# Kernel optimization log

Measured on AMD Instinct MI355X. Metric: run time of the kernel, lower is better.

Reference implementation:

```python
import jax, jax.numpy as jnp
import numpy as np

B, T, C, U = 256, 1024, 128, 100   # batch, time, num_classes (incl. blank), max label len
BLANK = C - 1                      # TF/Keras CTC: blank is the LAST class
NEG = -1.0e30                      # log-space -inf surrogate (fp32-safe)
EPS = 1e-7                         # keras backend epsilon used in ctc_batch_cost


def setup_inputs() -> dict:
    key = jax.random.key(0)
    k1, k2, k3 = jax.random.split(key, 3)
    # ctc_batch_cost consumes post-softmax probabilities
    logits = jax.random.normal(k1, (B, T, C), dtype=jnp.float32)
    y_pred = jax.nn.softmax(logits, axis=-1)
    y_true = jax.random.randint(k2, (B, U), 0, BLANK)          # labels in [0, C-2]
    label_len = jax.random.randint(k3, (B,), 1, U + 1)         # 1..U
    return {"y_pred": y_pred, "y_true": y_true, "label_len": label_len}


def _ctc_batch_cost(y_pred, y_true, label_len):
    # log probs, matching keras: log(prob + epsilon)
    logp = jnp.log(y_pred + EPS)                               # [B,T,C]
    S = 2 * U + 1
    # extended label sequence: blank, l1, blank, l2, ..., blank
    ext = jnp.full((B, S), BLANK, dtype=y_true.dtype)
    ext = ext.at[:, 1::2].set(y_true)                          # [B,S]
    # skip (s-2 -> s) allowed iff ext[s] != blank and ext[s] != ext[s-2]
    can_skip = jnp.concatenate(
        [jnp.zeros((B, 2), dtype=bool),
         (ext[:, 2:] != BLANK) & (ext[:, 2:] != ext[:, :-2])], axis=1)  # [B,S]

    logp_t = jnp.transpose(logp, (1, 0, 2))                    # [T,B,C]
    # t = 0 init: only s=0 (blank) and s=1 (first label) reachable
    lp0 = jnp.take_along_axis(logp_t[0], ext, axis=1)          # [B,S]
    alpha0 = jnp.full((B, S), NEG, dtype=logp.dtype)
    alpha0 = alpha0.at[:, 0].set(lp0[:, 0]).at[:, 1].set(lp0[:, 1])

    def step(alpha, lp_c):
        # lp_c: [B,C] log probs at time t; gather per extended-label position
        lp = jnp.take_along_axis(lp_c, ext, axis=1)            # [B,S]
        a1 = jnp.pad(alpha[:, :-1], ((0, 0), (1, 0)), constant_values=NEG)
        a2 = jnp.pad(alpha[:, :-2], ((0, 0), (2, 0)), constant_values=NEG)
        a2 = jnp.where(can_skip, a2, NEG)
        alpha = jax.nn.logsumexp(jnp.stack([alpha, a1, a2]), axis=0) + lp
        return alpha, None

    alpha, _ = jax.lax.scan(step, alpha0, logp_t[1:])          # [B,S]
    # total log-likelihood ends at s = 2L-1 (last label) or s = 2L (trailing blank)
    end = 2 * label_len[:, None]                               # [B,1]
    a_end = jnp.take_along_axis(alpha, jnp.concatenate([end - 1, end], axis=1), axis=1)
    return -jax.nn.logsumexp(a_end, axis=1, keepdims=True)     # [B,1] per-example loss


def reference(y_pred, y_true, label_len):
    # matches tf.keras.backend.ctc_batch_cost(y_true, y_pred, fill(T), label_len)
    return _ctc_batch_cost(y_pred, y_true, label_len)
```

## Files before the change

kernel.cpp:

```cpp
#include <hip/hip_runtime.h>


#define Bc 256
#define Tc 1024
#define Cc 128
#define Uc 100
#define BLANKc 127
#define EPSc 1e-7f
#define LN2f 0.69314718055994530942f
#define RSTRIDE 130
#define NSLOT 128
#define SLOTB (NSLOT*RSTRIDE*4)
#define QD 8

__global__ __launch_bounds__(64) void ctc_skew_kernel(
    const float* __restrict__ y_pred,
    const int*   __restrict__ y_true,
    const int*   __restrict__ label_len,
    float*       __restrict__ out)
{
    __shared__ __align__(16) float rowbuf[NSLOT * RSTRIDE];
    __shared__ float shA[204];
    __shared__ int   shE[64];

    const int b    = blockIdx.x;
    const int lane = threadIdx.x;
    const float* gp = y_pred + (size_t)b * (Tc * Cc);
    char* rb = (char*)rowbuf;

    const int k0  = 2*lane, k1 = 2*lane+1;
    const int k0c = k0 < Uc ? k0 : Uc-1;
    const int k1c = k1 < Uc ? k1 : Uc-1;
    const int y0  = y_true[b*Uc + k0c];
    const int y1  = y_true[b*Uc + k1c];
    int ym1 = y0;
    if (lane > 0) ym1 = y_true[b*Uc + k0 - 1];
    const float ms1 = (lane > 0 && y0 != ym1) ? 1.0f : 0.0f;
    const float ms3 = (y1 != y0) ? 1.0f : 0.0f;
    const float mh  = (lane > 0) ? 1.0f : 0.0f;
    const int y0b = y0 * 4, y1b = y1 * 4;

    float a0=0.f, a1=0.f, a2=0.f, a3=0.f;
    if (lane == 0) { a0 = gp[BLANKc]+EPSc; a1 = gp[y0]+EPSc; }
    int e = 0;

    {
        const float4 z = make_float4(0.f, 0.f, 0.f, 0.f);
        float4* rb4 = (float4*)rowbuf;
#pragma unroll
        for (int i = 0; i < 65; ++i) rb4[i*64 + lane] = z;
    }

#pragma unroll
    for (int i = 0; i < 8; ++i) {
        const int f4  = i*64 + lane;
        const int row = f4 >> 5;
        const int c4  = (f4 & 31) * 4;
        float4 v = *(const float4*)(gp + row*Cc + c4);
        float* dst = &rowbuf[row*RSTRIDE + c4];
        dst[0]=v.x+EPSc; dst[1]=v.y+EPSc; dst[2]=v.z+EPSc; dst[3]=v.w+EPSc;
    }

    float2 Q[QD];
#pragma unroll
    for (int k = 0; k < QD; ++k)
        Q[k] = *(const float2*)(gp + (16+k)*Cc + lane*2);

    int swb = (((1 - lane) & (NSLOT-1)) * RSTRIDE - RSTRIDE) * 4;
    if (swb < 0) swb += SLOTB;
    int wswb = 15 * RSTRIDE * 4;
    const int lane8 = lane * 8;

    float q2a = 0.f, q1a = 0.f;
    int ELa = 0, ELb = 0;

    auto body = [&](int n, int j, bool fzp) {
        swb += RSTRIDE*4; if (swb >= SLOTB) swb -= SLOTB;
        const float pb = *(const float*)(rb + swb + BLANKc*4);
        const float p0 = *(const float*)(rb + swb + y0b);
        const float p1 = *(const float*)(rb + swb + y1b);
        wswb += RSTRIDE*4; if (wswb >= SLOTB) wswb -= SLOTB;
        float2 qv = Q[j & 7];
        qv.x += EPSc; qv.y += EPSc;
        *(float2*)(rb + wswb + lane8) = qv;
        int lr = n + 23; lr = lr > Tc-1 ? Tc-1 : lr;
        Q[j & 7] = *(const float2*)(gp + lr*Cc + lane*2);
        const int el = ((j == 0) || (j >= 5 && j <= 8) || (j >= 13)) ? ELb : ELa;
        const float h1r = q2a; q2a = q1a;
        int d = el - e; d = d > 126 ? 126 : d;
        const float h1 = mh * ldexpf(h1r, d);
        const float n0 = (a0 + h1) * pb;
        const float n1 = (a1 + a0 + ms1*h1) * p0;
        const float n2 = (a2 + a1) * pb;
        const float n3 = (a3 + a2 + ms3*a1) * p1;
        bool upd = true;
        if (fzp) upd = (lane >= n - (Tc-1));
        if (upd) { a0=n0; a1=n1; a2=n2; a3=n3; }
        if ((j & 3) == 3) {
            const float m = fmaxf(fmaxf(a0,a1), fmaxf(a2,a3));
            int ex = (int)((__float_as_uint(m) >> 23) & 0xFF) - 127;
            ex = (m > 0.0f) ? ex : (el - e);
            a0 = ldexpf(a0,-ex); a1 = ldexpf(a1,-ex);
            a2 = ldexpf(a2,-ex); a3 = ldexpf(a3,-ex);
            e += ex;
        }
        q1a = __shfl_up(a3, 1, 64);
        if ((j & 3) == 3) {
            const int es = __shfl_up(e, 1, 64);
            if (j == 3 || j == 11) ELb = es; else ELa = es;
        }
    };

    int n = 1;
    for (int c = 0; c < 63; ++c) {
#pragma unroll
        for (int j = 0; j < 16; ++j) { body(n, j, false); ++n; }
    }
    for (int c = 0; c < 4; ++c) {
#pragma unroll
        for (int j = 0; j < 16; ++j) { body(n, j, true); ++n; }
    }
    body(n, 0, true);

    if (lane < 51) {
        shA[4*lane+0] = a0; shA[4*lane+1] = a1;
        shA[4*lane+2] = a2; shA[4*lane+3] = a3;
        shE[lane] = e;
    }
    __syncthreads();
    if (lane == 0) {
        const int L  = label_len[b];
        const int s1 = 2*L - 1, s2 = 2*L;
        const float v1 = shA[s1], v2 = shA[s2];
        const int   e1 = shE[s1 >> 2], e2 = shE[s2 >> 2];
        const int   em = e1 > e2 ? e1 : e2;
        const float sum = ldexpf(v1, e1-em) + ldexpf(v2, e2-em);
        const float r   = __log2f(sum) + (float)em;
        out[b] = -LN2f * r;
    }
}

extern "C" void kernel_launch(void* const* d_in, const int* in_sizes, int n_in,
                              void* d_out, int out_size, void* d_ws, size_t ws_size,
                              hipStream_t stream) {
    const float* y_pred    = (const float*)d_in[0];
    const int*   y_true    = (const int*)d_in[1];
    const int*   label_len = (const int*)d_in[2];
    float*       out       = (float*)d_out;
    ctc_skew_kernel<<<Bc, 64, 0, stream>>>(y_pred, y_true, label_len, out);
}
```

Before: 252.0 us.

## Process two time steps per iteration with a two-step lane skew

The wavefront schedule changes so that each lane lags its neighbour by two time steps instead of one. Each iteration then computes two recurrence steps back to back, with one cross-lane shuffle between them, and renormalises once per pair. The exponent and shifted-alpha history registers are restructured to match. The row ring buffer grows to 160 slots and the prefetch queue to 16 rows to cover the larger skew. This aims to halve per-step shuffle, exponent and ring-index overhead on the serial dependency chain, at the cost of more LDS, more registers and a longer drain phase.

```diff
diff --git a/kernel.cpp b/kernel.cpp
--- a/kernel.cpp
+++ b/kernel.cpp
@@ -9,11 +9,12 @@
 #define EPSc 1e-7f
 #define LN2f 0.69314718055994530942f
 #define RSTRIDE 130
-#define NSLOT 128
-#define SLOTB (NSLOT*RSTRIDE*4)
-#define QD 8
+#define NSLOT 160
+#define RSB (RSTRIDE*4)
+#define SLOTB (NSLOT*RSB)
+#define QD 16
 
-__global__ __launch_bounds__(64) void ctc_skew_kernel(
+__global__ __launch_bounds__(64) void ctc_pair_kernel(
     const float* __restrict__ y_pred,
     const int*   __restrict__ y_true,
     const int*   __restrict__ label_len,
@@ -39,20 +40,22 @@
     const float ms3 = (y1 != y0) ? 1.0f : 0.0f;
     const float mh  = (lane > 0) ? 1.0f : 0.0f;
     const int y0b = y0 * 4, y1b = y1 * 4;
+    const int lane2 = lane * 2, lane8 = lane * 8;
 
     float a0=0.f, a1=0.f, a2=0.f, a3=0.f;
     if (lane == 0) { a0 = gp[BLANKc]+EPSc; a1 = gp[y0]+EPSc; }
     int e = 0;
 
     {
-        const float4 z = make_float4(0.f, 0.f, 0.f, 0.f);
+        const float4 z = make_float4(0.f,0.f,0.f,0.f);
         float4* rb4 = (float4*)rowbuf;
 #pragma unroll
-        for (int i = 0; i < 65; ++i) rb4[i*64 + lane] = z;
+        for (int i = 0; i < 81; ++i) rb4[i*64 + lane] = z;
+        if (lane < 16) rb4[81*64 + lane] = z;
     }
 
 #pragma unroll
-    for (int i = 0; i < 8; ++i) {
+    for (int i = 0; i < 9; ++i) {
         const int f4  = i*64 + lane;
         const int row = f4 >> 5;
         const int c4  = (f4 & 31) * 4;
@@ -64,39 +67,61 @@
     float2 Q[QD];
 #pragma unroll
     for (int k = 0; k < QD; ++k)
-        Q[k] = *(const float2*)(gp + (16+k)*Cc + lane*2);
+        Q[k] = *(const float2*)(gp + (18+k)*Cc + lane2);
 
-    int swb = (((1 - lane) & (NSLOT-1)) * RSTRIDE - RSTRIDE) * 4;
-    if (swb < 0) swb += SLOTB;
-    int wswb = 15 * RSTRIDE * 4;
-    const int lane8 = lane * 8;
+    int r0 = 1 - lane2; r0 %= NSLOT; if (r0 < 0) r0 += NSLOT;
+    int sprev = r0*RSB - RSB; if (sprev < 0) sprev += SLOTB;
+    int wprev = 16*RSB;
+    int n2 = 2;
 
-    float q2a = 0.f, q1a = 0.f;
-    int ELa = 0, ELb = 0;
+    float hA1 = 0.f, hB1 = 0.f, hB2 = 0.f;
+    int   eL1 = 0,   eL2 = 0;
 
-    auto body = [&](int n, int j, bool fzp) {
-        swb += RSTRIDE*4; if (swb >= SLOTB) swb -= SLOTB;
-        const float pb = *(const float*)(rb + swb + BLANKc*4);
-        const float p0 = *(const float*)(rb + swb + y0b);
-        const float p1 = *(const float*)(rb + swb + y1b);
-        wswb += RSTRIDE*4; if (wswb >= SLOTB) wswb -= SLOTB;
-        float2 qv = Q[j & 7];
-        qv.x += EPSc; qv.y += EPSc;
-        *(float2*)(rb + wswb + lane8) = qv;
-        int lr = n + 23; lr = lr > Tc-1 ? Tc-1 : lr;
-        Q[j & 7] = *(const float2*)(gp + lr*Cc + lane*2);
-        const int el = ((j == 0) || (j >= 5 && j <= 8) || (j >= 13)) ? ELb : ELa;
-        const float h1r = q2a; q2a = q1a;
+    auto iter = [&](int j, bool fzp) {
+        int s1 = sprev + RSB; if (s1 >= SLOTB) s1 -= SLOTB;
+        int s2 = s1 + RSB;    if (s2 >= SLOTB) s2 -= SLOTB;
+        sprev = s2;
+        const float pb1 = *(const float*)(rb + s1 + BLANKc*4);
+        const float p01 = *(const float*)(rb + s1 + y0b);
+        const float p11 = *(const float*)(rb + s1 + y1b);
+        const float pb2 = *(const float*)(rb + s2 + BLANKc*4);
+        const float p02 = *(const float*)(rb + s2 + y0b);
+        const float p12 = *(const float*)(rb + s2 + y1b);
+        int w1 = wprev + 2*RSB; if (w1 >= SLOTB) w1 -= SLOTB;
+        int w2 = w1 + RSB;      if (w2 >= SLOTB) w2 -= SLOTB;
+        wprev = w1;
+        float2 qa = Q[2*j], qb = Q[2*j+1];
+        qa.x += EPSc; qa.y += EPSc; qb.x += EPSc; qb.y += EPSc;
+        *(float2*)(rb + w1 + lane8) = qa;
+        *(float2*)(rb + w2 + lane8) = qb;
+        int lr1 = n2 + 32; lr1 = lr1 > Tc-1 ? Tc-1 : lr1;
+        int lr2 = n2 + 33; lr2 = lr2 > Tc-1 ? Tc-1 : lr2;
+        Q[2*j]   = *(const float2*)(gp + lr1*Cc + lane2);
+        Q[2*j+1] = *(const float2*)(gp + lr2*Cc + lane2);
+        const int el = eL2;
         int d = el - e; d = d > 126 ? 126 : d;
-        const float h1 = mh * ldexpf(h1r, d);
-        const float n0 = (a0 + h1) * pb;
-        const float n1 = (a1 + a0 + ms1*h1) * p0;
-        const float n2 = (a2 + a1) * pb;
-        const float n3 = (a3 + a2 + ms3*a1) * p1;
-        bool upd = true;
-        if (fzp) upd = (lane >= n - (Tc-1));
-        if (upd) { a0=n0; a1=n1; a2=n2; a3=n3; }
-        if ((j & 3) == 3) {
+        const float h1 = mh * ldexpf(hB2, d);
+        const float h2 = mh * ldexpf(hA1, d);
+        {
+            const float n0 = (a0 + h1) * pb1;
+            const float n1 = (a1 + a0 + ms1*h1) * p01;
+            const float nv = (a2 + a1) * pb1;
+            const float n3 = (a3 + a2 + ms3*a1) * p11;
+            bool upd = true;
+            if (fzp) upd = (lane2 >= n2 - 1024);
+            if (upd) { a0=n0; a1=n1; a2=nv; a3=n3; }
+        }
+        const float haNew = __shfl_up(a3, 1, 64);
+        {
+            const float n0 = (a0 + h2) * pb2;
+            const float n1 = (a1 + a0 + ms1*h2) * p02;
+            const float nv = (a2 + a1) * pb2;
+            const float n3 = (a3 + a2 + ms3*a1) * p12;
+            bool upd = true;
+            if (fzp) upd = (lane2 >= n2 - 1023);
+            if (upd) { a0=n0; a1=n1; a2=nv; a3=n3; }
+        }
+        {
             const float m = fmaxf(fmaxf(a0,a1), fmaxf(a2,a3));
             int ex = (int)((__float_as_uint(m) >> 23) & 0xFF) - 127;
             ex = (m > 0.0f) ? ex : (el - e);
@@ -104,23 +129,20 @@
             a2 = ldexpf(a2,-ex); a3 = ldexpf(a3,-ex);
             e += ex;
         }
-        q1a = __shfl_up(a3, 1, 64);
-        if ((j & 3) == 3) {
-            const int es = __shfl_up(e, 1, 64);
-            if (j == 3 || j == 11) ELb = es; else ELa = es;
-        }
+        hB2 = hB1; hB1 = __shfl_up(a3, 1, 64);
+        eL2 = eL1; eL1 = __shfl_up(e , 1, 64);
+        hA1 = haNew;
+        n2 += 2;
     };
 
-    int n = 1;
     for (int c = 0; c < 63; ++c) {
 #pragma unroll
-        for (int j = 0; j < 16; ++j) { body(n, j, false); ++n; }
+        for (int j = 0; j < 8; ++j) iter(j, false);
     }
-    for (int c = 0; c < 4; ++c) {
+    for (int c = 0; c < 8; ++c) {
 #pragma unroll
-        for (int j = 0; j < 16; ++j) { body(n, j, true); ++n; }
+        for (int j = 0; j < 8; ++j) iter(j, true);
     }
-    body(n, 0, true);
 
     if (lane < 51) {
         shA[4*lane+0] = a0; shA[4*lane+1] = a1;
@@ -147,5 +169,5 @@
     const int*   y_true    = (const int*)d_in[1];
     const int*   label_len = (const int*)d_in[2];
     float*       out       = (float*)d_out;
-    ctc_skew_kernel<<<Bc, 64, 0, stream>>>(y_pred, y_true, label_len, out);
+    ctc_pair_kernel<<<Bc, 64, 0, stream>>>(y_pred, y_true, label_len, out);
 }
```

Result: slower. 271.0 us (+7.6%).

## Gather per-lane label probabilities directly from global into compact LDS ring

Applied to the files above, without the earlier changes.

Instead of staging whole probability rows in shared memory and gathering three columns per step from LDS, each lane now gathers its blank/y0/y1 probabilities from global memory 16 rows ahead and stores them as a float4 in a per-lane slot ring. Reads from the ring are skewed by lane and prefetched 4 steps ahead into registers, so LDS traffic per step drops to one float4 write and one read. This trades coalesced float2 row loads for scattered 4-byte global gathers, uses more registers for the 16-deep queue, and replaces the two-register shuffle history with a 16-entry array.

```diff
diff --git a/kernel.cpp b/kernel.cpp
--- a/kernel.cpp
+++ b/kernel.cpp
@@ -8,25 +8,22 @@
 #define BLANKc 127
 #define EPSc 1e-7f
 #define LN2f 0.69314718055994530942f
-#define RSTRIDE 130
-#define NSLOT 128
-#define SLOTB (NSLOT*RSTRIDE*4)
-#define QD 8
+#define SLOTS 128
+#define QGD 16
 
-__global__ __launch_bounds__(64) void ctc_skew_kernel(
+__global__ __launch_bounds__(64) void ctc_vg_kernel(
     const float* __restrict__ y_pred,
     const int*   __restrict__ y_true,
     const int*   __restrict__ label_len,
     float*       __restrict__ out)
 {
-    __shared__ __align__(16) float rowbuf[NSLOT * RSTRIDE];
-    __shared__ float shA[204];
-    __shared__ int   shE[64];
+    __shared__ float4 pbuf[SLOTS][64];
+    __shared__ float  shA[204];
+    __shared__ int    shE[64];
 
     const int b    = blockIdx.x;
     const int lane = threadIdx.x;
     const float* gp = y_pred + (size_t)b * (Tc * Cc);
-    char* rb = (char*)rowbuf;
 
     const int k0  = 2*lane, k1 = 2*lane+1;
     const int k0c = k0 < Uc ? k0 : Uc-1;
@@ -38,64 +35,56 @@
     const float ms1 = (lane > 0 && y0 != ym1) ? 1.0f : 0.0f;
     const float ms3 = (y1 != y0) ? 1.0f : 0.0f;
     const float mh  = (lane > 0) ? 1.0f : 0.0f;
-    const int y0b = y0 * 4, y1b = y1 * 4;
 
     float a0=0.f, a1=0.f, a2=0.f, a3=0.f;
     if (lane == 0) { a0 = gp[BLANKc]+EPSc; a1 = gp[y0]+EPSc; }
     int e = 0;
 
-    {
-        const float4 z = make_float4(0.f, 0.f, 0.f, 0.f);
-        float4* rb4 = (float4*)rowbuf;
+    const float4 z4 = make_float4(0.f,0.f,0.f,0.f);
+    for (int s = 64; s < SLOTS; ++s) pbuf[s][lane] = z4;
+
+    for (int r = 0; r < 5; ++r) {
+        const float* rp = gp + r*Cc;
+        pbuf[r][lane] = make_float4(rp[BLANKc], rp[y0], rp[y1], 0.f);
+    }
+    float4 QG[QGD];
 #pragma unroll
-        for (int i = 0; i < 65; ++i) rb4[i*64 + lane] = z;
+    for (int k = 0; k < QGD; ++k) QG[k] = z4;
+    for (int r = 5; r <= 16; ++r) {
+        const float* rp = gp + r*Cc;
+        QG[r & 15] = make_float4(rp[BLANKc], rp[y0], rp[y1], 0.f);
     }
+    float4 PQ[4];
+#pragma unroll
+    for (int nc = 1; nc <= 4; ++nc)
+        PQ[nc & 3] = pbuf[(nc - lane) & (SLOTS-1)][lane];
 
+    float HQ[16];
 #pragma unroll
-    for (int i = 0; i < 8; ++i) {
-        const int f4  = i*64 + lane;
-        const int row = f4 >> 5;
-        const int c4  = (f4 & 31) * 4;
-        float4 v = *(const float4*)(gp + row*Cc + c4);
-        float* dst = &rowbuf[row*RSTRIDE + c4];
-        dst[0]=v.x+EPSc; dst[1]=v.y+EPSc; dst[2]=v.z+EPSc; dst[3]=v.w+EPSc;
-    }
-
-    float2 Q[QD];
-#pragma unroll
-    for (int k = 0; k < QD; ++k)
-        Q[k] = *(const float2*)(gp + (16+k)*Cc + lane*2);
-
-    int swb = (((1 - lane) & (NSLOT-1)) * RSTRIDE - RSTRIDE) * 4;
-    if (swb < 0) swb += SLOTB;
-    int wswb = 15 * RSTRIDE * 4;
-    const int lane8 = lane * 8;
-
-    float q2a = 0.f, q1a = 0.f;
+    for (int k = 0; k < 16; ++k) HQ[k] = 0.f;
     int ELa = 0, ELb = 0;
 
     auto body = [&](int n, int j, bool fzp) {
-        swb += RSTRIDE*4; if (swb >= SLOTB) swb -= SLOTB;
-        const float pb = *(const float*)(rb + swb + BLANKc*4);
-        const float p0 = *(const float*)(rb + swb + y0b);
-        const float p1 = *(const float*)(rb + swb + y1b);
-        wswb += RSTRIDE*4; if (wswb >= SLOTB) wswb -= SLOTB;
-        float2 qv = Q[j & 7];
-        qv.x += EPSc; qv.y += EPSc;
-        *(float2*)(rb + wswb + lane8) = qv;
-        int lr = n + 23; lr = lr > Tc-1 ? Tc-1 : lr;
-        Q[j & 7] = *(const float2*)(gp + lr*Cc + lane*2);
+        pbuf[(n + 4) & (SLOTS-1)][lane] = QG[(j + 5) & 15];
+        {
+            int rv = n + 16; rv = rv > Tc-1 ? Tc-1 : rv;
+            const float* rp = gp + rv * Cc;
+            QG[(j + 1) & 15] = make_float4(rp[BLANKc], rp[y0], rp[y1], 0.f);
+        }
+        const float4 pv = PQ[(j + 1) & 3];
+        const float pb = pv.x + EPSc, p0 = pv.y + EPSc, p1 = pv.z + EPSc;
+        PQ[(j + 1) & 3] = pbuf[(n + 4 - lane) & (SLOTS-1)][lane];
         const int el = ((j == 0) || (j >= 5 && j <= 8) || (j >= 13)) ? ELb : ELa;
-        const float h1r = q2a; q2a = q1a;
+        const float h1r = HQ[(j + 14) & 15];
         int d = el - e; d = d > 126 ? 126 : d;
         const float h1 = mh * ldexpf(h1r, d);
         const float n0 = (a0 + h1) * pb;
         const float n1 = (a1 + a0 + ms1*h1) * p0;
-        const float n2 = (a2 + a1) * pb;
+        const float nv = (a2 + a1) * pb;
         const float n3 = (a3 + a2 + ms3*a1) * p1;
         bool upd = true;
         if (fzp) upd = (lane >= n - (Tc-1));
-        if (upd) { a0=n0; a1=n1; a2=n2; a3=n3; }
+        if (upd) { a0=n0; a1=n1; a2=nv; a3=n3; }
         if ((j & 3) == 3) {
             const float m = fmaxf(fmaxf(a0,a1), fmaxf(a2,a3));
             int ex = (int)((__float_as_uint(m) >> 23) & 0xFF) - 127;
@@ -104,7 +93,7 @@
             a2 = ldexpf(a2,-ex); a3 = ldexpf(a3,-ex);
             e += ex;
         }
-        q1a = __shfl_up(a3, 1, 64);
+        HQ[j] = __shfl_up(a3, 1, 64);
         if ((j & 3) == 3) {
             const int es = __shfl_up(e, 1, 64);
             if (j == 3 || j == 11) ELb = es; else ELa = es;
@@ -147,5 +136,5 @@
     const int*   y_true    = (const int*)d_in[1];
     const int*   label_len = (const int*)d_in[2];
     float*       out       = (float*)d_out;
-    ctc_skew_kernel<<<Bc, 64, 0, stream>>>(y_pred, y_true, label_len, out);
+    ctc_vg_kernel<<<Bc, 64, 0, stream>>>(y_pred, y_true, label_len, out);
 }
```

After: 280.7 us. 1.11x slower.

## Software-pipeline LDS reads and lane shuffles with inline asm and manual waitcnt

Applied to the files above, without the earlier changes.

The per-timestep loop is rewritten in inline assembly so that the LDS probability reads for the next step and the lane-shift bpermute are issued one step ahead, using double-buffered A/B registers, with explicit s_waitcnt counters controlling completion. The EPS add moves from the global-to-LDS staging path to the point of use. The intent is to take LDS and cross-lane latency off the serial recurrence's critical path. In exchange, the hand-set waitcnt values and slot offsets must be exactly right, or the kernel will read stale data.

```diff
diff --git a/kernel.cpp b/kernel.cpp
--- a/kernel.cpp
+++ b/kernel.cpp
@@ -1,4 +1,5 @@
 #include <hip/hip_runtime.h>
+#include <stdint.h>
 
 
 #define Bc 256
@@ -9,11 +10,23 @@
 #define EPSc 1e-7f
 #define LN2f 0.69314718055994530942f
 #define RSTRIDE 130
+#define RSB (RSTRIDE*4)
 #define NSLOT 128
-#define SLOTB (NSLOT*RSTRIDE*4)
+#define SLOTB (NSLOT*RSB)
 #define QD 8
 
-__global__ __launch_bounds__(64) void ctc_skew_kernel(
+typedef __attribute__((address_space(3))) float LDSF;
+
+#define DSREAD(dst, ad) \
+    asm volatile("ds_read_b32 %0, %1" : "=v"(dst) : "v"(ad) : "memory")
+#define DSWRITE64(ad, data) \
+    asm volatile("ds_write_b64 %0, %1" :: "v"(ad), "v"(data) : "memory")
+#define BPERM(dst, idx, src) \
+    asm volatile("ds_bpermute_b32 %0, %1, %2" : "=v"(dst) : "v"(idx), "v"(src) : "memory")
+#define GLOAD2(dst, ptr) \
+    asm volatile("global_load_dwordx2 %0, %1, off" : "=v"(dst) : "v"(ptr) : "memory")
+
+__global__ __launch_bounds__(64) void ctc_asm_kernel(
     const float* __restrict__ y_pred,
     const int*   __restrict__ y_true,
     const int*   __restrict__ label_len,
@@ -26,7 +39,6 @@
     const int b    = blockIdx.x;
     const int lane = threadIdx.x;
     const float* gp = y_pred + (size_t)b * (Tc * Cc);
-    char* rb = (char*)rowbuf;
 
     const int k0  = 2*lane, k1 = 2*lane+1;
     const int k0c = k0 < Uc ? k0 : Uc-1;
@@ -38,17 +50,23 @@
     const float ms1 = (lane > 0 && y0 != ym1) ? 1.0f : 0.0f;
     const float ms3 = (y1 != y0) ? 1.0f : 0.0f;
     const float mh  = (lane > 0) ? 1.0f : 0.0f;
-    const int y0b = y0 * 4, y1b = y1 * 4;
+    const uint32_t y0B = (uint32_t)y0 << 2;
+    const uint32_t y1B = (uint32_t)y1 << 2;
+    const uint32_t BLB = (uint32_t)BLANKc << 2;
+    const int lane2 = lane * 2;
+    const uint32_t lane8 = (uint32_t)lane * 8u;
 
     float a0=0.f, a1=0.f, a2=0.f, a3=0.f;
     if (lane == 0) { a0 = gp[BLANKc]+EPSc; a1 = gp[y0]+EPSc; }
     int e = 0;
 
+    const uint32_t rb0 = (uint32_t)(uintptr_t)(LDSF*)rowbuf;
+
     {
-        const float4 z = make_float4(0.f, 0.f, 0.f, 0.f);
-        float4* rb4 = (float4*)rowbuf;
+        const float4 z = make_float4(0.f,0.f,0.f,0.f);
+        float4* r4p = (float4*)rowbuf;
 #pragma unroll
-        for (int i = 0; i < 65; ++i) rb4[i*64 + lane] = z;
+        for (int i = 0; i < 65; ++i) r4p[i*64 + lane] = z;
     }
 
 #pragma unroll
@@ -56,46 +74,54 @@
         const int f4  = i*64 + lane;
         const int row = f4 >> 5;
         const int c4  = (f4 & 31) * 4;
-        float4 v = *(const float4*)(gp + row*Cc + c4);
+        const float4 v = *(const float4*)(gp + row*Cc + c4);
         float* dst = &rowbuf[row*RSTRIDE + c4];
-        dst[0]=v.x+EPSc; dst[1]=v.y+EPSc; dst[2]=v.z+EPSc; dst[3]=v.w+EPSc;
+        dst[0]=v.x; dst[1]=v.y; dst[2]=v.z; dst[3]=v.w;
     }
 
-    float2 Q[QD];
+    uint64_t Q[QD];
 #pragma unroll
     for (int k = 0; k < QD; ++k)
-        Q[k] = *(const float2*)(gp + (16+k)*Cc + lane*2);
+        GLOAD2(Q[k], gp + (16+k)*Cc + lane2);
 
-    int swb = (((1 - lane) & (NSLOT-1)) * RSTRIDE - RSTRIDE) * 4;
+    float pqbA, pq0A, pq1A, pqbB, pq0B, pq1B;
+    float hqA = 0.f, hqB = 0.f;
+    int   ELa = 0,  ELb = 0;
+    const uint32_t up4 = (uint32_t)((lane > 0 ? lane-1 : 0) * 4);
+
+    asm volatile("s_waitcnt lgkmcnt(0)" ::: "memory");
+    {
+        const uint32_t s1 = rb0 + (((uint32_t)(1 - lane)) & 127u) * RSB;
+        const uint32_t s2 = rb0 + (((uint32_t)(2 - lane)) & 127u) * RSB;
+        DSREAD(pqbA, s1 + BLB); DSREAD(pq0A, s1 + y0B); DSREAD(pq1A, s1 + y1B);
+        DSREAD(pqbB, s2 + BLB); DSREAD(pq0B, s2 + y0B); DSREAD(pq1B, s2 + y1B);
+    }
+    asm volatile("s_waitcnt vmcnt(0) lgkmcnt(0)" ::: "memory");
+    __builtin_amdgcn_sched_barrier(0);
+
+    int swb = (int)((((uint32_t)(3 - lane)) & 127u) * RSB) - RSB;
     if (swb < 0) swb += SLOTB;
-    int wswb = 15 * RSTRIDE * 4;
-    const int lane8 = lane * 8;
-
-    float q2a = 0.f, q1a = 0.f;
-    int ELa = 0, ELb = 0;
+    int wswb = 15 * RSB;
 
     auto body = [&](int n, int j, bool fzp) {
-        swb += RSTRIDE*4; if (swb >= SLOTB) swb -= SLOTB;
-        const float pb = *(const float*)(rb + swb + BLANKc*4);
-        const float p0 = *(const float*)(rb + swb + y0b);
-        const float p1 = *(const float*)(rb + swb + y1b);
-        wswb += RSTRIDE*4; if (wswb >= SLOTB) wswb -= SLOTB;
-        float2 qv = Q[j & 7];
-        qv.x += EPSc; qv.y += EPSc;
-        *(float2*)(rb + wswb + lane8) = qv;
-        int lr = n + 23; lr = lr > Tc-1 ? Tc-1 : lr;
-        Q[j & 7] = *(const float2*)(gp + lr*Cc + lane*2);
-        const int el = ((j == 0) || (j >= 5 && j <= 8) || (j >= 13)) ? ELb : ELa;
-        const float h1r = q2a; q2a = q1a;
+        asm volatile("s_waitcnt lgkmcnt(5)" ::: "memory");
+        __builtin_amdgcn_sched_barrier(0);
+        const bool sA = ((j & 1) == 0);
+        const float pbr = sA ? pqbA : pqbB;
+        const float p0r = sA ? pq0A : pq0B;
+        const float p1r = sA ? pq1A : pq1B;
+        const float h1r = sA ? hqA  : hqB;
+        const int   el  = ((j == 0) || (j >= 5 && j <= 8) || (j >= 13)) ? ELb : ELa;
+        const float pb = pbr + EPSc, p0 = p0r + EPSc, p1 = p1r + EPSc;
         int d = el - e; d = d > 126 ? 126 : d;
         const float h1 = mh * ldexpf(h1r, d);
         const float n0 = (a0 + h1) * pb;
         const float n1 = (a1 + a0 + ms1*h1) * p0;
-        const float n2 = (a2 + a1) * pb;
+        const float nv = (a2 + a1) * pb;
         const float n3 = (a3 + a2 + ms3*a1) * p1;
         bool upd = true;
         if (fzp) upd = (lane >= n - (Tc-1));
-        if (upd) { a0=n0; a1=n1; a2=n2; a3=n3; }
+        if (upd) { a0=n0; a1=n1; a2=nv; a3=n3; }
         if ((j & 3) == 3) {
             const float m = fmaxf(fmaxf(a0,a1), fmaxf(a2,a3));
             int ex = (int)((__float_as_uint(m) >> 23) & 0xFF) - 127;
@@ -104,10 +130,19 @@
             a2 = ldexpf(a2,-ex); a3 = ldexpf(a3,-ex);
             e += ex;
         }
-        q1a = __shfl_up(a3, 1, 64);
+        wswb += RSB; if (wswb >= SLOTB) wswb -= SLOTB;
+        asm volatile("s_waitcnt vmcnt(7)" ::: "memory");
+        DSWRITE64(rb0 + (uint32_t)wswb + lane8, Q[j & 7]);
+        int lr = n + 23; lr = lr > Tc-1 ? Tc-1 : lr;
+        GLOAD2(Q[j & 7], gp + lr*Cc + lane2);
+        swb += RSB; if (swb >= SLOTB) swb -= SLOTB;
+        const uint32_t ga = rb0 + (uint32_t)swb;
+        if (sA) { DSREAD(pqbA, ga + BLB); DSREAD(pq0A, ga + y0B); DSREAD(pq1A, ga + y1B); }
+        else    { DSREAD(pqbB, ga + BLB); DSREAD(pq0B, ga + y0B); DSREAD(pq1B, ga + y1B); }
+        if (sA) { BPERM(hqA, up4, a3); } else { BPERM(hqB, up4, a3); }
         if ((j & 3) == 3) {
-            const int es = __shfl_up(e, 1, 64);
-            if (j == 3 || j == 11) ELb = es; else ELa = es;
+            if (j == 3 || j == 11) { BPERM(ELb, up4, e); }
+            else                   { BPERM(ELa, up4, e); }
         }
     };
 
@@ -121,6 +156,9 @@
         for (int j = 0; j < 16; ++j) { body(n, j, true); ++n; }
     }
     body(n, 0, true);
+
+    asm volatile("s_waitcnt vmcnt(0) lgkmcnt(0)" ::: "memory");
+    __builtin_amdgcn_sched_barrier(0);
 
     if (lane < 51) {
         shA[4*lane+0] = a0; shA[4*lane+1] = a1;
@@ -147,5 +185,5 @@
     const int*   y_true    = (const int*)d_in[1];
     const int*   label_len = (const int*)d_in[2];
     float*       out       = (float*)d_out;
-    ctc_skew_kernel<<<Bc, 64, 0, stream>>>(y_pred, y_true, label_len, out);
+    ctc_asm_kernel<<<Bc, 64, 0, stream>>>(y_pred, y_true, label_len, out);
 }
```

Result: slower. 258.1 us (+2.4%).
